# Kernel optimization log

Hardware: AMD Instinct MI355X
Metric: run time of the kernel (lower is better)

Reference implementation:

```python
import jax, jax.numpy as jnp
import numpy as np

NUM_EXPERTS = 64
K = 8
LOAD_BALANCE_SCALE = 0.01
NOISY_STD = 1.0

def setup_inputs() -> dict:
    key = jax.random.key(0)
    k1, k2, k3, k4 = jax.random.split(key, 4)
    N, D, E = 32768, 1024, NUM_EXPERTS
    return {
        "x_flat": jax.random.normal(k1, (N, D), dtype=jnp.float32),
        "gate_w": jax.random.normal(k2, (E, D), dtype=jnp.float32) * (1.0 / np.sqrt(D)),
        "noise_weight": jax.random.normal(k3, (E,), dtype=jnp.float32) * 0.02,
        "noise": jax.random.normal(k4, (N, E), dtype=jnp.float32),
    }

def reference(x_flat, gate_w, noise_weight, noise):
    E = gate_w.shape[0]
    # gate logits: [N, E]
    logits = jnp.einsum('nd,ed->ne', x_flat, gate_w)
    gate_weights = jax.nn.softmax(logits, axis=-1)
    gate_weights_mean = gate_weights.mean(axis=0)  # [E]
    uniform = jnp.full_like(gate_weights_mean, 1.0 / E)
    load_balance_loss = jnp.mean((gate_weights_mean - uniform) ** 2) * LOAD_BALANCE_SCALE
    # noisy logits; noise ~ randn, scaled per-expert by noise_weight
    logits_noisy = logits + (noise * NOISY_STD) * noise_weight
    top_k_vals, top_k_ids = jax.lax.top_k(logits_noisy, K)  # [N, K]
    # scatter top-k logits into -inf canvas, then softmax -> sparse gate weights
    rows = jnp.arange(logits.shape[0])[:, None]
    sparse = jnp.full_like(logits_noisy, -jnp.inf).at[rows, top_k_ids].set(top_k_vals)
    top_k_gated_weights = jax.nn.softmax(sparse, axis=-1)
    return (top_k_gated_weights, top_k_ids, load_balance_loss)
```

## Files before the change

### kernel.cpp

```cpp
#include <hip/hip_runtime.h>
#include <math.h>

#define N_ROWS 32768
#define DIM    1024
#define NE     64
#define KTOP   8


extern "C" __global__ void __launch_bounds__(512, 4)
moe_gate_kernel(const float* __restrict__ x, const float* __restrict__ gw,
                const float* __restrict__ nw, const float* __restrict__ noise,
                float* __restrict__ out0, float* __restrict__ out1,
                float* __restrict__ lossp,
                double* __restrict__ esum, int* __restrict__ ticket) {
    __shared__ __align__(16) float smem[8512];
    __shared__ int isLast;
    float* xt  = smem;
    float* wt  = smem + 4096;
    float* red = smem;
    float* lg  = smem + 4352;

    const int tid  = threadIdx.x;
    const int lane = tid & 63;
    const int wid  = __builtin_amdgcn_readfirstlane(tid >> 6);
    const int er   = lane >> 3;
    const int rr   = lane & 7;
    const int er8  = er * 8;
    const int rr8  = rr * 8;
    const int row0 = blockIdx.x * 64;
    const int kwb  = wid * 128;

    float acc[8][8];
#pragma unroll
    for (int m = 0; m < 8; ++m)
#pragma unroll
        for (int n = 0; n < 8; ++n) acc[m][n] = 0.f;

    const float* gx   = x  + (size_t)(row0 + lane) * DIM + kwb;
    const float* gwp  = gw + (size_t)lane * DIM + kwb;
    float*       ws_x = xt + wid * 512 + lane;
    float*       ws_w = wt + wid * 512 + lane;
    const float* rd_x = xt + wid * 512 + rr8;
    const float* rd_w = wt + wid * 512 + er8;

    float px[8], pw[8];
    *(float4*)(px + 0) = *(const float4*)(gx + 0);
    *(float4*)(px + 4) = *(const float4*)(gx + 4);
    *(float4*)(pw + 0) = *(const float4*)(gwp + 0);
    *(float4*)(pw + 4) = *(const float4*)(gwp + 4);
#pragma unroll
    for (int q = 0; q < 8; ++q) {
        ws_x[q * 64] = px[q];
        ws_w[q * 64] = pw[q];
    }

#pragma unroll 1
    for (int rnd = 0; rnd < 16; ++rnd) {
        const int nxt = (rnd < 15) ? (rnd + 1) * 8 : 15 * 8;
        *(float4*)(px + 0) = *(const float4*)(gx  + nxt + 0);
        *(float4*)(px + 4) = *(const float4*)(gx  + nxt + 4);
        *(float4*)(pw + 0) = *(const float4*)(gwp + nxt + 0);
        *(float4*)(pw + 4) = *(const float4*)(gwp + nxt + 4);
        __builtin_amdgcn_sched_barrier(0);

#pragma unroll 1
        for (int q = 0; q < 8; ++q) {
            float xf[8], wf[8];
            *(float4*)(xf + 0) = *(const float4*)(rd_x + q * 64 + 0);
            *(float4*)(xf + 4) = *(const float4*)(rd_x + q * 64 + 4);
            *(float4*)(wf + 0) = *(const float4*)(rd_w + q * 64 + 0);
            *(float4*)(wf + 4) = *(const float4*)(rd_w + q * 64 + 4);
#pragma unroll
            for (int m = 0; m < 8; ++m)
#pragma unroll
                for (int n = 0; n < 8; ++n)
                    acc[m][n] = fmaf(xf[m], wf[n], acc[m][n]);
        }

#pragma unroll
        for (int q = 0; q < 8; ++q) {
            ws_x[q * 64] = px[q];
            ws_w[q * 64] = pw[q];
        }
    }

    __syncthreads();
#pragma unroll
    for (int s = 0; s < 8; ++s) {
        float4 v0 = make_float4(acc[s][0], acc[s][1], acc[s][2], acc[s][3]);
        float4 v1 = make_float4(acc[s][4], acc[s][5], acc[s][6], acc[s][7]);
        *(float4*)(red + wid * 544 + rr * 68 + er8 + 0) = v0;
        *(float4*)(red + wid * 544 + rr * 68 + er8 + 4) = v1;
        __syncthreads();
        {
            const int r2 = tid >> 6, e = tid & 63;
            float t = 0.f;
#pragma unroll
            for (int w = 0; w < 8; ++w) t += red[w * 544 + r2 * 68 + e];
            lg[(r2 * 8 + s) * 65 + e] = t;
        }
        __syncthreads();
    }

    const float nwl = nw[lane];
    float epart = 0.f;

#pragma unroll 1
    for (int i = 0; i < 8; ++i) {
        const int    lrow = wid * 8 + i;
        const size_t grow = (size_t)(row0 + lrow);
        const float  lgv  = lg[lrow * 65 + lane];

        float m = lgv;
#pragma unroll
        for (int off = 32; off; off >>= 1) m = fmaxf(m, __shfl_xor(m, off));
        float p = __expf(lgv - m);
        float s = p;
#pragma unroll
        for (int off = 32; off; off >>= 1) s += __shfl_xor(s, off);
        epart += p / s;

        const float nz    = noise[grow * NE + lane];
        const float noisy = fmaf(nz, nwl, lgv);
        float cur  = noisy;
        bool  sel  = false;
        float mtop = 0.f;
        int   myid = 0;
#pragma unroll
        for (int j = 0; j < KTOP; ++j) {
            float v = cur; int id = lane;
#pragma unroll
            for (int off = 32; off; off >>= 1) {
                float ov = __shfl_xor(v, off);
                int   oi = __shfl_xor(id, off);
                if (ov > v || (ov == v && oi < id)) { v = ov; id = oi; }
            }
            if (j == 0) mtop = v;
            if (lane == id) { sel = true; cur = -INFINITY; }
            if (lane == j) myid = id;
        }

        float swv  = sel ? __expf(noisy - mtop) : 0.f;
        float ssum = swv;
#pragma unroll
        for (int off = 32; off; off >>= 1) ssum += __shfl_xor(ssum, off);

        out0[grow * NE + lane] = swv / ssum;
        if (lane < KTOP) out1[grow * KTOP + lane] = (float)myid;
    }

    __syncthreads();
    red[wid * 64 + lane] = epart;
    __syncthreads();
    if (tid < NE) {
        float t = 0.f;
#pragma unroll
        for (int w = 0; w < 8; ++w) t += red[w * 64 + tid];
        atomicAdd(&esum[tid], (double)t);
        __threadfence();
    }
    __syncthreads();
    if (tid == 0) {
        int t = atomicAdd(ticket, 1);
        isLast = (t == (int)gridDim.x - 1);
        __threadfence();
    }
    __syncthreads();

    if (isLast && tid < NE) {
        double v = atomicAdd(&esum[tid], 0.0);
        double mean = v * (1.0 / 32768.0);
        double d  = mean - (1.0 / 64.0);
        double sq = d * d;
#pragma unroll
        for (int off = 32; off; off >>= 1) sq += __shfl_xor(sq, off);
        if (tid == 0) lossp[0] = (float)(sq * (1.0 / 64.0) * 0.01);
    }
}

extern "C" void kernel_launch(void* const* d_in, const int* in_sizes, int n_in,
                              void* d_out, int out_size, void* d_ws, size_t ws_size,
                              hipStream_t stream) {
    const float* x     = (const float*)d_in[0];
    const float* gw    = (const float*)d_in[1];
    const float* nw    = (const float*)d_in[2];
    const float* noise = (const float*)d_in[3];

    float* out0  = (float*)d_out;
    float* out1  = out0 + (size_t)N_ROWS * NE;
    float* lossp = out1 + (size_t)N_ROWS * KTOP;

    double* esum   = (double*)d_ws;
    int*    ticket = (int*)((char*)d_ws + 512);

    hipMemsetAsync(d_ws, 0, 520, stream);
    moe_gate_kernel<<<N_ROWS / 64, 512, 0, stream>>>(x, gw, nw, noise,
                                                     out0, out1, lossp, esum, ticket);
}
```

Before: 291.3 us.

## Split gate GEMM across K into four blocks with atomic logits, separate epilogue kernel

Splits the fused kernel in two. A GEMM kernel with four times as many blocks partitions the 1024-wide reduction into four quarters, and each block atomically adds its partial logits into out0 after out0 is zeroed by a memset. A second kernel reads those logits back from global memory to do the softmax, noisy top-k, sparse softmax and the load-balance loss. This raises parallelism (2048 blocks instead of 512) but drops the register double-buffered prefetch, and it adds a full-size memset, float atomics, a global round trip of the logits and an extra launch.

```diff
diff --git a/kernel.cpp b/kernel.cpp
--- a/kernel.cpp
+++ b/kernel.cpp
@@ -8,17 +8,12 @@
 
 
 extern "C" __global__ void __launch_bounds__(512, 4)
-moe_gate_kernel(const float* __restrict__ x, const float* __restrict__ gw,
-                const float* __restrict__ nw, const float* __restrict__ noise,
-                float* __restrict__ out0, float* __restrict__ out1,
-                float* __restrict__ lossp,
-                double* __restrict__ esum, int* __restrict__ ticket) {
-    __shared__ __align__(16) float smem[8512];
-    __shared__ int isLast;
+moe_gemm_kernel(const float* __restrict__ x, const float* __restrict__ gw,
+                float* __restrict__ logits) {
+    __shared__ __align__(16) float smem[8192];
     float* xt  = smem;
     float* wt  = smem + 4096;
     float* red = smem;
-    float* lg  = smem + 4352;
 
     const int tid  = threadIdx.x;
     const int lane = tid & 63;
@@ -27,8 +22,10 @@
     const int rr   = lane & 7;
     const int er8  = er * 8;
     const int rr8  = rr * 8;
-    const int row0 = blockIdx.x * 64;
-    const int kwb  = wid * 128;
+    const int rg   = blockIdx.x >> 2;
+    const int kq   = blockIdx.x & 3;
+    const int row0 = rg * 64;
+    const int kwb  = kq * 256 + wid * 32;
 
     float acc[8][8];
 #pragma unroll
@@ -43,26 +40,20 @@
     const float* rd_x = xt + wid * 512 + rr8;
     const float* rd_w = wt + wid * 512 + er8;
 
-    float px[8], pw[8];
-    *(float4*)(px + 0) = *(const float4*)(gx + 0);
-    *(float4*)(px + 4) = *(const float4*)(gx + 4);
-    *(float4*)(pw + 0) = *(const float4*)(gwp + 0);
-    *(float4*)(pw + 4) = *(const float4*)(gwp + 4);
-#pragma unroll
-    for (int q = 0; q < 8; ++q) {
-        ws_x[q * 64] = px[q];
-        ws_w[q * 64] = pw[q];
-    }
-
 #pragma unroll 1
-    for (int rnd = 0; rnd < 16; ++rnd) {
-        const int nxt = (rnd < 15) ? (rnd + 1) * 8 : 15 * 8;
-        *(float4*)(px + 0) = *(const float4*)(gx  + nxt + 0);
-        *(float4*)(px + 4) = *(const float4*)(gx  + nxt + 4);
-        *(float4*)(pw + 0) = *(const float4*)(gwp + nxt + 0);
-        *(float4*)(pw + 4) = *(const float4*)(gwp + nxt + 4);
-        __builtin_amdgcn_sched_barrier(0);
-
+    for (int rnd = 0; rnd < 4; ++rnd) {
+        {
+            float px[8], pw[8];
+            *(float4*)(px + 0) = *(const float4*)(gx  + rnd * 8 + 0);
+            *(float4*)(px + 4) = *(const float4*)(gx  + rnd * 8 + 4);
+            *(float4*)(pw + 0) = *(const float4*)(gwp + rnd * 8 + 0);
+            *(float4*)(pw + 4) = *(const float4*)(gwp + rnd * 8 + 4);
+#pragma unroll
+            for (int q = 0; q < 8; ++q) {
+                ws_x[q * 64] = px[q];
+                ws_w[q * 64] = pw[q];
+            }
+        }
 #pragma unroll 1
         for (int q = 0; q < 8; ++q) {
             float xf[8], wf[8];
@@ -75,12 +66,6 @@
 #pragma unroll
                 for (int n = 0; n < 8; ++n)
                     acc[m][n] = fmaf(xf[m], wf[n], acc[m][n]);
-        }
-
-#pragma unroll
-        for (int q = 0; q < 8; ++q) {
-            ws_x[q * 64] = px[q];
-            ws_w[q * 64] = pw[q];
         }
     }
 
@@ -97,10 +82,24 @@
             float t = 0.f;
 #pragma unroll
             for (int w = 0; w < 8; ++w) t += red[w * 544 + r2 * 68 + e];
-            lg[(r2 * 8 + s) * 65 + e] = t;
+            atomicAdd(&logits[(size_t)(row0 + r2 * 8 + s) * NE + e], t);
         }
         __syncthreads();
     }
+}
+
+extern "C" __global__ void __launch_bounds__(512, 4)
+moe_epi_kernel(const float* __restrict__ nw, const float* __restrict__ noise,
+               float* __restrict__ out0, float* __restrict__ out1,
+               float* __restrict__ lossp,
+               double* __restrict__ esum, int* __restrict__ ticket) {
+    __shared__ float red[8 * 64];
+    __shared__ int isLast;
+
+    const int tid  = threadIdx.x;
+    const int lane = tid & 63;
+    const int wid  = __builtin_amdgcn_readfirstlane(tid >> 6);
+    const int row0 = blockIdx.x * 64;
 
     const float nwl = nw[lane];
     float epart = 0.f;
@@ -109,7 +108,7 @@
     for (int i = 0; i < 8; ++i) {
         const int    lrow = wid * 8 + i;
         const size_t grow = (size_t)(row0 + lrow);
-        const float  lgv  = lg[lrow * 65 + lane];
+        const float  lgv  = out0[grow * NE + lane];
 
         float m = lgv;
 #pragma unroll
@@ -194,6 +193,8 @@
     int*    ticket = (int*)((char*)d_ws + 512);
 
     hipMemsetAsync(d_ws, 0, 520, stream);
-    moe_gate_kernel<<<N_ROWS / 64, 512, 0, stream>>>(x, gw, nw, noise,
-                                                     out0, out1, lossp, esum, ticket);
+    hipMemsetAsync(out0, 0, (size_t)N_ROWS * NE * sizeof(float), stream);
+    moe_gemm_kernel<<<N_ROWS / 64 * 4, 512, 0, stream>>>(x, gw, out0);
+    moe_epi_kernel<<<N_ROWS / 64, 512, 0, stream>>>(nw, noise, out0, out1,
+                                                    lossp, esum, ticket);
 }
```

Result: slower. 329.0 us (+13.0%).
